# Kernel optimization log

Measured on AMD Instinct MI355X. Metric: run time of the kernel, lower is better.

The kernel has to match this reference:

```python
import jax, jax.numpy as jnp
import numpy as np

H, O, M, D, B = 4, 32, 128, 16, 1024
JITTER = 1e-4


def k_rbf(theta, X, Y):
    # theta: [H, 1+D] (log sf2, log lengthscales); X: [O,Mx,D]; Y: [O,My,D]
    sf2 = jnp.exp(theta[:, 0])[:, None, None, None]          # [H,1,1,1]
    ls = jnp.exp(theta[:, 1:])                               # [H,D]
    Xs = X[None] / ls[:, None, None, :]                      # [H,O,Mx,D]
    Ys = Y[None] / ls[:, None, None, :]                      # [H,O,My,D]
    d2 = ((Xs ** 2).sum(-1)[..., :, None]
          + (Ys ** 2).sum(-1)[..., None, :]
          - 2.0 * jnp.einsum('homd,hond->homn', Xs, Ys))
    return sf2 * jnp.exp(-0.5 * jnp.maximum(d2, 0.0))


def vec2tril(vec, m):
    r, c = jnp.tril_indices(m)
    L = jnp.zeros(vec.shape[:-1] + (m, m), vec.dtype)
    return L.at[..., r, c].set(vec)


def _st(Lmat, rhs):
    return jax.scipy.linalg.solve_triangular(Lmat, rhs, lower=True)


def setup_inputs() -> dict:
    key = jax.random.key(0)
    ks = jax.random.split(key, 8)
    eye = jnp.eye(M, dtype=jnp.float32)
    return {
        'x': jax.random.normal(ks[0], (B, D), jnp.float32),
        'z': 0.5 * jax.random.normal(ks[1], (O, M, D), jnp.float32),
        'u_mean': 0.5 * jax.random.normal(ks[2], (O, M, 1), jnp.float32),
        'u_tril_vec': 0.1 * jax.random.normal(ks[3], (O, M * (M + 1) // 2), jnp.float32),
        'm_old': 0.5 * jax.random.normal(ks[4], (O, M, 1), jnp.float32),
        'L_old': jnp.tril(0.1 * jax.random.normal(ks[5], (O, M, M), jnp.float32)) + eye,
        'z_old': 0.5 * jax.random.normal(ks[6], (O, M, D), jnp.float32),
        'theta': 0.1 * jax.random.normal(ks[7], (H, D + 1), jnp.float32),
    }


def reference(x, z, u_mean, u_tril_vec, m_old, L_old, z_old, theta):
    dt = x.dtype
    u_tril = vec2tril(u_tril_vec, M)                          # [O,M,M]
    eyeM = jnp.eye(M, dtype=dt)

    # ---- linear_gauss_joint (one previous task) ----
    kuf = k_rbf(theta, z_old, z)                              # [H,O,M,M]
    kuu = k_rbf(theta, z_old, z_old)                          # [H,O,M,M]
    Lkuu = jnp.linalg.cholesky(kuu + JITTER * eyeM)
    LKinvKuf = _st(Lkuu, kuf)
    m_oldh = jnp.broadcast_to(m_old[None], (H, O, M, 1))
    L_oldh = jnp.broadcast_to(L_old[None], (H, O, M, M))
    LKinvm = _st(Lkuu, m_oldh)
    Am = jnp.einsum('...ij,...ik->...jk', LKinvKuf, LKinvm)   # A @ m_old, [H,O,M,1]
    m_new = Am + u_mean[None]
    m_joint = jnp.concatenate([m_oldh, m_new], axis=-2)       # [H,O,2M,1]

    S_old = jnp.einsum('...ji,...ki->...jk', L_oldh, L_oldh)
    LKinvLS = _st(Lkuu, L_oldh)
    AtX = jnp.einsum('...ij,...ik->...jk', LKinvLS, LKinvKuf)  # [H,O,M,M]
    SoldAt = jnp.einsum('...ji,...ik->...jk', L_oldh, AtX)
    ASoldt = jnp.swapaxes(SoldAt, -1, -2)
    S_cur = jnp.einsum('...ji,...ki->...jk', u_tril, u_tril)[None]
    ASoldAt = jnp.einsum('...ij,...ik->...jk', AtX, AtX)
    cov_joint = jnp.concatenate([
        jnp.concatenate([S_old, SoldAt], axis=-1),
        jnp.concatenate([ASoldt, S_cur + ASoldAt], axis=-1)], axis=-2)
    eye2M = jnp.eye(2 * M, dtype=dt)
    L_joint = jnp.linalg.cholesky(cov_joint + JITTER * eye2M)  # [H,O,2M,2M]
    z_joint = jnp.concatenate([z_old, z], axis=-2)             # [O,2M,D]

    # ---- linear_gauss_conditional_diag ----
    xb = jnp.broadcast_to(x[None], (O, B, D))
    kuf2 = k_rbf(theta, z_joint, xb)                           # [H,O,2M,B]
    kuu2 = k_rbf(theta, z_joint, z_joint)
    Lk2 = jnp.linalg.cholesky(kuu2 + JITTER * eye2M)
    LKinvu = _st(Lk2, m_joint)
    LKinvKuf2 = _st(Lk2, kuf2)
    kff_diag = jnp.exp(theta[:, 0])[:, None, None]             # [H,1,1]
    diag1 = (LKinvKuf2 ** 2).sum(axis=-2)                      # [H,O,B]
    LKinvLs = _st(Lk2, L_joint)
    vec2 = jnp.einsum('...ij,...ik->...jk', LKinvLs, LKinvKuf2)
    diag2 = (vec2 ** 2).sum(axis=-2)
    mu = jnp.einsum('...ij,...ik->...jk', LKinvKuf2, LKinvu)[..., 0]
    var = kff_diag - diag1 + diag2
    return mu, var
```

## Files before the change

kernel.cpp:

```cpp
#include <hip/hip_runtime.h>

#define H_ 4
#define O_ 32
#define HO 128
#define M_ 128
#define M2 256
#define D_ 16
#define B_ 1024
#define JIT 1e-4f

typedef unsigned short ushort_t;
typedef __bf16 v8bf __attribute__((ext_vector_type(8)));
typedef float v16f __attribute__((ext_vector_type(16)));
typedef unsigned short v8us __attribute__((ext_vector_type(8)));
typedef unsigned short v4us __attribute__((ext_vector_type(4)));

__device__ inline void splitbf(float v, ushort_t& hb, ushort_t& lb) {
    unsigned int u = __float_as_uint(v);
    hb = (ushort_t)(u >> 16);
    float hf = __uint_as_float((unsigned int)hb << 16);
    float r = v - hf;
    lb = (ushort_t)(__float_as_uint(r) >> 16);
}
__device__ inline float bf2f(ushort_t u) { return __uint_as_float((unsigned int)u << 16); }

__device__ __forceinline__ float rdlane(float v, int l) {
    return __int_as_float(__builtin_amdgcn_readlane(__float_as_int(v), l));
}

__device__ __forceinline__ int ro_(int i) {
    int M = i >> 2, k = i & 3;
    return 4 * (M + 1) * (2 * M + k);
}

__global__ __launch_bounds__(256) void k_prekuu2(const float* __restrict__ theta,
                                                 const float* __restrict__ x,
                                                 const float* __restrict__ z,
                                                 const float* __restrict__ z_old,
                                                 float* __restrict__ SF2,
                                                 float* __restrict__ XS, float* __restrict__ XN,
                                                 float* __restrict__ ZS, float* __restrict__ ZN,
                                                 float* __restrict__ K2) {
    int bb = blockIdx.x, t = threadIdx.x;
    __shared__ float zs[M2][D_];
    __shared__ float zn[M2];
    __shared__ float ls[D_];
    if (bb == 272) {
        if (t < H_) SF2[t] = __expf(theta[t * (D_ + 1)]);
        return;
    }
    if (bb >= 256) {
        int j = (bb - 256) * 256 + t;
        int h = j >> 10, b = j & 1023;
        if (t < D_) ls[t] = __expf(-theta[h * (D_ + 1) + 1 + t]);
        __syncthreads();
        float s = 0.f;
#pragma unroll
        for (int d = 0; d < D_; d++) {
            float v = x[b * D_ + d] * ls[d];
            XS[(long)j * D_ + d] = v;
            s += v * v;
        }
        XN[j] = s;
        return;
    }
    int pair = bb >> 1, half = bb & 1;
    int h = pair >> 5, o = pair & 31, i = t;
    if (t < D_) ls[t] = __expf(-theta[h * (D_ + 1) + 1 + t]);
    __syncthreads();
    const float* src = (i < M_) ? (z_old + ((long)o * M_ + i) * D_)
                                : (z + ((long)o * M_ + (i - M_)) * D_);
    float s = 0.f;
#pragma unroll
    for (int d = 0; d < D_; d++) {
        float v = src[d] * ls[d];
        zs[i][d] = v;
        if (half == 0) ZS[((long)pair * M2 + i) * D_ + d] = v;
        s += v * v;
    }
    zn[i] = s;
    if (half == 0) ZN[pair * M2 + i] = s;
    __syncthreads();
    float sf2 = __expf(theta[h * (D_ + 1)]);
    float my[D_];
#pragma unroll
    for (int d = 0; d < D_; d++) my[d] = zs[i][d];
    float myn = zn[i];
    int q0 = half * 128;
    for (int q = q0; q < q0 + 128; q++) {
        float dot = 0.f;
#pragma unroll
        for (int d = 0; d < D_; d++) dot += zs[q][d] * my[d];
        float d2 = fmaxf(zn[q] + myn - 2.f * dot, 0.f);
        float v = sf2 * __expf(-0.5f * d2);
        if (q == i) v += JIT;
        K2[(long)pair * M2 * M2 + (long)q * M2 + i] = v;
    }
}

#define AP_SZ 8448
#define LV_SZ 16896
#define WS_SZ 4608
#define TM_SZ 3456
#define SH_TOTAL (AP_SZ + LV_SZ + WS_SZ + TM_SZ + 128)

__device__ __forceinline__ void choltri_body(const float* __restrict__ S, int ldsrc,
                                             float* __restrict__ Li, long b1, int t,
                                             float* __restrict__ Ap, float* __restrict__ Lv,
                                             float* __restrict__ Ws4, float* __restrict__ Tm,
                                             float* __restrict__ rdia) {
#pragma unroll
    for (int u = 0; u < 16; u++) {
        int idx = u * 256 + t;
        int i = idx >> 5, jc = (idx & 31) * 4;
        float4 v = *(const float4*)(S + (long)i * ldsrc + jc);
        int tb = ro_(i) + jc;
        if (jc + 3 <= i) {
            *(float4*)&Ap[tb] = v;
        } else if (jc <= i) {
            Ap[tb] = v.x;
            if (jc + 1 <= i) Ap[tb + 1] = v.y;
            if (jc + 2 <= i) Ap[tb + 2] = v.z;
        }
    }
    __syncthreads();

    int lane = t & 63;
    int wav = t >> 6;
    int r = lane & 31;

    for (int kb = 0; kb < 4; kb++) {
        int c0 = kb * 32;
        if (wav == 0) {
            float a[32];
            int gr = c0 + r;
            int base = ro_(gr) + c0;
#pragma unroll
            for (int j = 0; j < 32; j++) a[j] = Ap[base + j];
#pragma unroll
            for (int k = 0; k < 32; k++) {
                float dk = rdlane(a[k], k);
                float rs = rsqrtf(dk);
                rs = rs * (1.5f - 0.5f * dk * rs * rs);
                a[k] *= rs;
                if (lane == k) rdia[c0 + k] = rs;
#pragma unroll
                for (int j = k + 1; j < 32; j++) {
                    float ljk = rdlane(a[k], j);
                    a[j] = fmaf(-a[k], ljk, a[j]);
                }
            }
            if (lane < 32) {
#pragma unroll
                for (int j = 0; j < 32; j++)
                    if (j <= r) Ap[base + j] = a[j];
            }
        }
        __syncthreads();
        int R = 96 - c0;
        if (R > 0) {
            if (t < R) {
                int gi = c0 + 32 + t;
                int pb = ro_(gi) + c0;
                float xr[32];
#pragma unroll
                for (int j = 0; j < 32; j++) xr[j] = Ap[pb + j];
#pragma unroll
                for (int q = 0; q < 32; q++) {
                    float xq = xr[q] * rdia[c0 + q];
                    xr[q] = xq;
#pragma unroll
                    for (int j = q + 1; j < 32; j++)
                        xr[j] = fmaf(-xq, Ap[ro_(c0 + j) + c0 + q], xr[j]);
                }
#pragma unroll
                for (int j = 0; j < 32; j++) Ap[pb + j] = xr[j];
            }
            __syncthreads();
            int nb = R >> 2;
            int ntile = nb * (nb + 1) / 2;
            for (int tp = t; tp < ntile; tp += 256) {
                int bi = (int)((sqrtf(8.f * tp + 1.f) - 1.f) * 0.5f);
                while ((bi + 1) * (bi + 2) / 2 <= tp) bi++;
                while (bi * (bi + 1) / 2 > tp) bi--;
                int bj = tp - bi * (bi + 1) / 2;
                int i0 = c0 + 32 + bi * 4, j0 = c0 + 32 + bj * 4;
                int ra[4], rb[4];
#pragma unroll
                for (int q = 0; q < 4; q++) {
                    ra[q] = ro_(i0 + q) + c0;
                    rb[q] = ro_(j0 + q) + c0;
                }
                float acc[4][4] = {};
#pragma unroll
                for (int k4 = 0; k4 < 8; k4++) {
                    float4 av[4], bv[4];
#pragma unroll
                    for (int q = 0; q < 4; q++) {
                        av[q] = *(const float4*)&Ap[ra[q] + k4 * 4];
                        bv[q] = *(const float4*)&Ap[rb[q] + k4 * 4];
                    }
#pragma unroll
                    for (int q = 0; q < 4; q++)
#pragma unroll
                        for (int rr = 0; rr < 4; rr++)
                            acc[q][rr] += av[q].x * bv[rr].x + av[q].y * bv[rr].y +
                                          av[q].z * bv[rr].z + av[q].w * bv[rr].w;
                }
#pragma unroll
                for (int q = 0; q < 4; q++)
#pragma unroll
                    for (int rr = 0; rr < 4; rr++) {
                        int gi = i0 + q, gj = j0 + rr;
                        if (gj <= gi) Ap[ro_(gi) + gj] -= acc[q][rr];
                    }
            }
            __syncthreads();
        }
    }

    {
        int pb = wav;
        int c0 = pb * 32;
        float a[32];
        int gr = c0 + r;
        int base = ro_(gr) + c0;
#pragma unroll
        for (int j = 0; j < 32; j++) a[j] = Ap[base + j];
        float wr[32];
#pragma unroll
        for (int i = 0; i < 32; i++) {
            float rdi = rdia[c0 + i];
            float acc = 0.f;
#pragma unroll
            for (int j = 0; j < i; j++) {
                float lij = rdlane(a[j], i);
                acc = fmaf(lij, wr[j], acc);
            }
            wr[i] = (i == r) ? rdi : -acc * rdi;
        }
        if (lane < 32) {
            float* Wp = Ws4 + pb * 1152;
#pragma unroll
            for (int i = 0; i < 32; i++) Wp[i * 36 + r] = wr[i];
        }
    }
    __syncthreads();

    for (int e = t; e < 4096; e += 256) {
        int i = e >> 5, j = (e & 31) * 4;
        int bi = i >> 5, bj = j >> 5;
        float4 v = make_float4(0.f, 0.f, 0.f, 0.f);
        if (bi == bj) v = *(const float4*)&Ws4[bi * 1152 + (i & 31) * 36 + (j & 31)];
        *(float4*)&Lv[i * 132 + j] = v;
    }
    __syncthreads();
    for (int d = 1; d < 4; d++) {
        int nblk = 4 - d;
        int ne = nblk * 256;
        for (int p = t; p < ne; p += 256) {
            int b = p >> 8, rc = p & 255;
            int rr = rc >> 3, c4 = (rc & 7) * 4;
            int ib = b + d;
            int abase = ro_(ib * 32 + rr);
            float4 acc = make_float4(0.f, 0.f, 0.f, 0.f);
            for (int k = b; k < ib; k++) {
                const float* Arow = Ap + abase + k * 32;
                const float* L0 = Lv + (k * 32) * 132 + b * 32 + c4;
#pragma unroll
                for (int q4 = 0; q4 < 8; q4++) {
                    float4 ar = *(const float4*)(Arow + q4 * 4);
                    const float* Lq = L0 + (q4 * 4) * 132;
                    float4 l0 = *(const float4*)(Lq);
                    float4 l1 = *(const float4*)(Lq + 132);
                    float4 l2 = *(const float4*)(Lq + 264);
                    float4 l3 = *(const float4*)(Lq + 396);
                    acc.x += ar.x * l0.x + ar.y * l1.x + ar.z * l2.x + ar.w * l3.x;
                    acc.y += ar.x * l0.y + ar.y * l1.y + ar.z * l2.y + ar.w * l3.y;
                    acc.z += ar.x * l0.z + ar.y * l1.z + ar.z * l2.z + ar.w * l3.z;
                    acc.w += ar.x * l0.w + ar.y * l1.w + ar.z * l2.w + ar.w * l3.w;
                }
            }
            *(float4*)(Tm + b * 1152 + rr * 36 + c4) = acc;
        }
        __syncthreads();
        for (int p = t; p < ne; p += 256) {
            int b = p >> 8, rc = p & 255;
            int rr = rc >> 3, c4 = (rc & 7) * 4;
            int ib = b + d;
            const float* Wp = Ws4 + ib * 1152 + rr * 36;
            const float* T0 = Tm + b * 1152 + c4;
            float4 acc = make_float4(0.f, 0.f, 0.f, 0.f);
#pragma unroll
            for (int q4 = 0; q4 < 8; q4++) {
                float4 w4 = *(const float4*)(Wp + q4 * 4);
                const float* Tq = T0 + (q4 * 4) * 36;
                float4 t0 = *(const float4*)(Tq);
                float4 t1 = *(const float4*)(Tq + 36);
                float4 t2 = *(const float4*)(Tq + 72);
                float4 t3 = *(const float4*)(Tq + 108);
                acc.x += w4.x * t0.x + w4.y * t1.x + w4.z * t2.x + w4.w * t3.x;
                acc.y += w4.x * t0.y + w4.y * t1.y + w4.z * t2.y + w4.w * t3.y;
                acc.z += w4.x * t0.z + w4.y * t1.z + w4.z * t2.z + w4.w * t3.z;
                acc.w += w4.x * t0.w + w4.y * t1.w + w4.z * t2.w + w4.w * t3.w;
            }
            *(float4*)(Lv + (ib * 32 + rr) * 132 + b * 32 + c4) =
                make_float4(-acc.x, -acc.y, -acc.z, -acc.w);
        }
        __syncthreads();
    }
#pragma unroll
    for (int u = 0; u < 16; u++) {
        int idx = u * 256 + t;
        int i = idx >> 5, jc = (idx & 31) * 4;
        *(float4*)(Li + b1 + (long)i * 128 + jc) = *(const float4*)(Lv + i * 132 + jc);
    }
}

__global__ __launch_bounds__(256) void k_choltri_tl(const float* __restrict__ src,
                                                    float* __restrict__ Li,
                                                    const float* __restrict__ L_old,
                                                    const float* __restrict__ vec,
                                                    ushort_t* __restrict__ WTh,
                                                    ushort_t* __restrict__ WTl) {
    int bb = blockIdx.x, t = threadIdx.x;
    __shared__ __align__(16) float SH[SH_TOTAL];
    if (bb < 128) {
        choltri_body(src + (long)bb * ((long)M2 * M2), M2, Li, (long)bb * 16384, t,
                     SH, SH + AP_SZ, SH + AP_SZ + LV_SZ, SH + AP_SZ + LV_SZ + WS_SZ,
                     SH + AP_SZ + LV_SZ + WS_SZ + TM_SZ);
        return;
    }
    int pair = bb - 128, o = pair & 31;
    long b2 = (long)pair * 65536;
    float* vs = SH;
    float(*tile)[33] = (float(*)[33])(SH + AP_SZ);
    for (int e = t; e < M_ * (M_ + 1) / 2; e += 256) vs[e] = vec[(long)o * (M_ * (M_ + 1) / 2) + e];
    __syncthreads();
    for (int e = t; e < 16384; e += 256) {
        int n = e >> 7, k = e & 127;
        float v = (k >= n) ? vs[k * (k + 1) / 2 + n] : 0.f;
        ushort_t hb, lb;
        splitbf(v, hb, lb);
        long a = b2 + (long)(128 + n) * 256 + 128 + k;
        WTh[a] = hb;
        WTl[a] = lb;
    }
    for (int e = t; e < 16384; e += 256) {
        int n = e >> 7, k = e & 127;
        long a = b2 + (long)(128 + n) * 256 + k;
        WTh[a] = 0;
        WTl[a] = 0;
    }
    const float* sp = L_old + (long)o * 16384;
    int tx = t & 31, ty = t >> 5;
    for (int bi = 0; bi < 4; bi++)
        for (int bj = 0; bj < 4; bj++) {
            __syncthreads();
            for (int r = ty; r < 32; r += 8)
                tile[r][tx] = sp[(long)(bi * 32 + r) * 128 + bj * 32 + tx];
            __syncthreads();
            for (int r = ty; r < 32; r += 8) {
                ushort_t hb, lb;
                splitbf(tile[tx][r], hb, lb);
                long a = b2 + (long)(bj * 32 + r) * 256 + bi * 32 + tx;
                WTh[a] = hb;
                WTl[a] = lb;
            }
        }
}

__global__ __launch_bounds__(256) void k_choltri_br(const float* __restrict__ src,
                                                    float* __restrict__ Li,
                                                    const float* __restrict__ A1,
                                                    const float* __restrict__ Linv1,
                                                    float* __restrict__ T1g,
                                                    const float* __restrict__ BLW,
                                                    ushort_t* __restrict__ LTh,
                                                    ushort_t* __restrict__ LTl,
                                                    ushort_t* __restrict__ WTh,
                                                    ushort_t* __restrict__ WTl) {
    int bb = blockIdx.x, t = threadIdx.x;
    __shared__ __align__(16) float SH[SH_TOTAL];
    if (bb < 128) {
        choltri_body(src + (long)bb * ((long)M2 * M2), M2, Li, (long)bb * 16384, t,
                     SH, SH + AP_SZ, SH + AP_SZ + LV_SZ, SH + AP_SZ + LV_SZ + WS_SZ,
                     SH + AP_SZ + LV_SZ + WS_SZ + TM_SZ);
        return;
    }
    if (bb < 256) {
        int pair = bb - 128;
        long b1 = (long)pair * 16384;
        float(*As)[132] = (float(*)[132])(SH + AP_SZ);
        float(*Bs)[132] = ((float(*)[132])(SH + AP_SZ)) + 16;
        const float* Apt = A1 + b1;
        const float* Bpt = Linv1 + b1;
        float* Cp = T1g + (long)pair * 65536;
        int tx = t & 15, ty = t >> 4;
        float acc[8][8] = {};
        for (int kt = 0; kt < M_; kt += 16) {
#pragma unroll
            for (int q = 0; q < 8; q++) {
                int e = q * 256 + t;
                int kk = e >> 7, m = e & 127;
                As[kk][m] = Apt[(long)(kt + kk) * 128 + m];
                Bs[kk][m] = Bpt[(long)(kt + kk) * 128 + m];
            }
            __syncthreads();
#pragma unroll
            for (int kk = 0; kk < 16; kk++) {
                float a[8], b[8];
#pragma unroll
                for (int q = 0; q < 8; q++) { a[q] = As[kk][ty + 16 * q]; b[q] = Bs[kk][tx + 16 * q]; }
#pragma unroll
                for (int q = 0; q < 8; q++)
#pragma unroll
                    for (int r = 0; r < 8; r++) acc[q][r] += a[q] * b[r];
            }
            __syncthreads();
        }
#pragma unroll
        for (int q = 0; q < 8; q++)
#pragma unroll
            for (int r = 0; r < 8; r++)
                Cp[(long)(ty + 16 * q) * 128 + tx + 16 * r] = acc[q][r];
        return;
    }
    if (bb < 384) {
        int pair = bb - 256;
        long b2 = (long)pair * 65536, b1 = (long)pair * 16384;
        float(*tile)[33] = (float(*)[33])(SH + AP_SZ);
        for (int e = t; e < 16384; e += 256) {
            int n = e >> 7, k = e & 127;
            long a = b2 + (long)(128 + n) * 256 + k;
            LTh[a] = 0;
            LTl[a] = 0;
        }
        const float* sp = Linv1 + b1;
        int tx = t & 31, ty = t >> 5;
        for (int bi = 0; bi < 4; bi++)
            for (int bj = 0; bj < 4; bj++) {
                __syncthreads();
                for (int r = ty; r < 32; r += 8)
                    tile[r][tx] = sp[(long)(bi * 32 + r) * 128 + bj * 32 + tx];
                __syncthreads();
                for (int r = ty; r < 32; r += 8) {
                    ushort_t hb, lb;
                    splitbf(tile[tx][r], hb, lb);
                    long a = b2 + (long)(bj * 32 + r) * 256 + bi * 32 + tx;
                    LTh[a] = hb;
                    LTl[a] = lb;
                }
            }
        return;
    }
    {
        int pair = bb - 384;
        long b2 = (long)pair * 65536, b1 = (long)pair * 16384;
        float(*tile)[33] = (float(*)[33])(SH + AP_SZ);
        const float* sp = BLW + b1;
        int tx = t & 31, ty = t >> 5;
        for (int bi = 0; bi < 4; bi++)
            for (int bj = 0; bj < 4; bj++) {
                __syncthreads();
                for (int r = ty; r < 32; r += 8)
                    tile[r][tx] = sp[(long)(bi * 32 + r) * 128 + bj * 32 + tx];
                __syncthreads();
                for (int r = ty; r < 32; r += 8) {
                    ushort_t hb, lb;
                    splitbf(tile[tx][r], hb, lb);
                    long a = b2 + (long)(bj * 32 + r) * 256 + 128 + bi * 32 + tx;
                    WTh[a] = hb;
                    WTl[a] = lb;
                }
            }
    }
}

__global__ __launch_bounds__(256) void k_a1a3(const float* __restrict__ Linv1,
                                              const float* __restrict__ KUU2,
                                              const float* __restrict__ L_old,
                                              float* __restrict__ A1, float* __restrict__ A3) {
    int pair = blockIdx.x, y = blockIdx.y, o = pair & 31;
    const float* Ap = Linv1 + (long)pair * 16384;
    const float* Bp = y ? (L_old + (long)o * 16384) : (KUU2 + (long)pair * 65536 + 128);
    int ldb = y ? 128 : 256;
    float* Cp = (y ? A3 : A1) + (long)pair * 16384;
    int t = threadIdx.x, tx = t & 15, ty = t >> 4;
    __shared__ float As[16][132], Bs[16][132];
    float acc[8][8] = {};
    for (int kt = 0; kt < M_; kt += 16) {
#pragma unroll
        for (int q = 0; q < 8; q++) {
            int e = q * 256 + t;
            int m = e >> 4, kk = e & 15;
            As[kk][m] = Ap[(long)m * 128 + kt + kk];
            int kk2 = e >> 7, n = e & 127;
            Bs[kk2][n] = Bp[(long)(kt + kk2) * ldb + n];
        }
        __syncthreads();
#pragma unroll
        for (int kk = 0; kk < 16; kk++) {
            float a[8], b[8];
#pragma unroll
            for (int q = 0; q < 8; q++) { a[q] = As[kk][ty + 16 * q]; b[q] = Bs[kk][tx + 16 * q]; }
#pragma unroll
            for (int q = 0; q < 8; q++)
#pragma unroll
                for (int r = 0; r < 8; r++) acc[q][r] += a[q] * b[r];
        }
        __syncthreads();
    }
#pragma unroll
    for (int q = 0; q < 8; q++)
#pragma unroll
        for (int r = 0; r < 8; r++)
            Cp[(long)(ty + 16 * q) * 128 + tx + 16 * r] = acc[q][r];
}

__global__ __launch_bounds__(256) void k_blwschur(const float* __restrict__ A1,
                                                  const float* __restrict__ A3,
                                                  float* __restrict__ BLW,
                                                  float* __restrict__ KUU2,
                                                  const float* __restrict__ Linv1,
                                                  const float* __restrict__ m_old,
                                                  const float* __restrict__ u_mean,
                                                  float* __restrict__ MJ,
                                                  float* __restrict__ CV) {
    int pair = blockIdx.x, y = blockIdx.y, o = pair & 31;
    int t = threadIdx.x;
    if (y == 2) {
        CV[pair * 256 + t] = 0.f;
        __shared__ float mo[128], a2[128];
        if (t < 128) mo[t] = m_old[o * 128 + t];
        __syncthreads();
        if (t < 128) {
            const float* Lr = Linv1 + (long)pair * 16384 + (long)t * 128;
            float acc = 0.f;
            for (int j = 0; j <= t; j++) acc += Lr[j] * mo[j];
            a2[t] = acc;
        }
        __syncthreads();
        if (t < 128) {
            float m = 0.f;
            for (int i = 0; i < 128; i++) m += A1[(long)pair * 16384 + (long)i * 128 + t] * a2[i];
            MJ[pair * 256 + t] = mo[t];
            MJ[pair * 256 + 128 + t] = m + u_mean[o * 128 + t];
        }
        return;
    }
    const float* Ap = A1 + (long)pair * 16384;
    const float* Bp = (y ? A1 : A3) + (long)pair * 16384;
    float* Cp;
    int ldc;
    if (y) { Cp = KUU2 + (long)pair * 65536 + 128L * 256 + 128; ldc = 256; }
    else   { Cp = BLW + (long)pair * 16384; ldc = 128; }
    int tx = t & 15, ty = t >> 4;
    __shared__ float As[16][132], Bs[16][132];
    float acc[8][8] = {};
    for (int kt = 0; kt < M_; kt += 16) {
#pragma unroll
        for (int q = 0; q < 8; q++) {
            int e = q * 256 + t;
            int kk = e >> 7, m = e & 127;
            As[kk][m] = Ap[(long)(kt + kk) * 128 + m];
            Bs[kk][m] = Bp[(long)(kt + kk) * 128 + m];
        }
        __syncthreads();
#pragma unroll
        for (int kk = 0; kk < 16; kk++) {
            float a[8], b[8];
#pragma unroll
            for (int q = 0; q < 8; q++) { a[q] = As[kk][ty + 16 * q]; b[q] = Bs[kk][tx + 16 * q]; }
#pragma unroll
            for (int q = 0; q < 8; q++)
#pragma unroll
                for (int r = 0; r < 8; r++) acc[q][r] += a[q] * b[r];
        }
        __syncthreads();
    }
#pragma unroll
    for (int q = 0; q < 8; q++)
#pragma unroll
        for (int r = 0; r < 8; r++) {
            long idx = (long)(ty + 16 * q) * ldc + tx + 16 * r;
            if (y) Cp[idx] -= acc[q][r];
            else Cp[idx] = acc[q][r];
        }
}

__global__ __launch_bounds__(256) void k_blicalc2(const float* __restrict__ Linv2,
                                                  const float* __restrict__ T1g,
                                                  ushort_t* __restrict__ LTh,
                                                  ushort_t* __restrict__ LTl) {
    int pair = blockIdx.x, y = blockIdx.y;
    int t = threadIdx.x, tx = t & 15, ty = t >> 4;
    long b1 = (long)pair * 16384, b2 = (long)pair * 65536;
    int m0 = y * 64;
    __shared__ float T1s[64][129];
    __shared__ float As[16][68], Bs[16][132];
    const float* Apt = Linv2 + b1;
    const float* Bpt = T1g + (long)pair * 65536;
    float acc[4][8] = {};
    for (int kt = 0; kt < M_; kt += 16) {
#pragma unroll
        for (int q = 0; q < 4; q++) {
            int e = q * 256 + t;
            int m = e >> 4, kk = e & 15;
            As[kk][m] = Apt[(long)(m0 + m) * 128 + kt + kk];
        }
#pragma unroll
        for (int q = 0; q < 8; q++) {
            int e = q * 256 + t;
            int kk2 = e >> 7, n = e & 127;
            Bs[kk2][n] = Bpt[(long)(kt + kk2) * 128 + n];
        }
        __syncthreads();
#pragma unroll
        for (int kk = 0; kk < 16; kk++) {
            float a[4], b[8];
#pragma unroll
            for (int q = 0; q < 4; q++) a[q] = As[kk][ty + 16 * q];
#pragma unroll
            for (int r = 0; r < 8; r++) b[r] = Bs[kk][tx + 16 * r];
#pragma unroll
            for (int q = 0; q < 4; q++)
#pragma unroll
                for (int r = 0; r < 8; r++) acc[q][r] += a[q] * b[r];
        }
        __syncthreads();
    }
#pragma unroll
    for (int q = 0; q < 4; q++)
#pragma unroll
        for (int r = 0; r < 8; r++) T1s[ty + 16 * q][tx + 16 * r] = -acc[q][r];
    __syncthreads();
    for (int e = t; e < 8192; e += 256) {
        int j = e >> 6, i2 = e & 63;
        ushort_t hb, lb;
        splitbf(T1s[i2][j], hb, lb);
        long a = b2 + (long)j * 256 + 128 + m0 + i2;
        LTh[a] = hb;
        LTl[a] = lb;
    }
    __syncthreads();
    for (int e = t; e < 8192; e += 256) {
        int k2 = e >> 7, j = e & 127;
        T1s[k2][j] = Apt[(long)(m0 + k2) * 128 + j];
    }
    __syncthreads();
    for (int e = t; e < 8192; e += 256) {
        int n = e >> 6, k2 = e & 63;
        ushort_t hb, lb;
        splitbf(T1s[k2][n], hb, lb);
        long a = b2 + (long)(128 + n) * 256 + 128 + m0 + k2;
        LTh[a] = hb;
        LTl[a] = lb;
    }
}

#define BSTR 56
template <int TILES3>
__global__ __launch_bounds__(256) void k_bmmx(const ushort_t* __restrict__ Ah,
                                              const ushort_t* __restrict__ Al,
                                              const ushort_t* __restrict__ Bh,
                                              const ushort_t* __restrict__ Bl,
                                              float* __restrict__ Cf,
                                              ushort_t* __restrict__ Chi,
                                              ushort_t* __restrict__ Clo,
                                              const float* __restrict__ Dm,
                                              int kLoMode, float alpha,
                                              const float* __restrict__ MJv,
                                              float* __restrict__ CVat) {
    int pair = blockIdx.x;
    long base = (long)pair * 65536;
    int I0, J0, mir = 0;
    if (TILES3) {
        int qb = blockIdx.y;
        I0 = (qb == 0) ? 0 : 128;
        J0 = (qb == 2) ? 0 : I0;
        mir = (qb == 2);
    } else {
        I0 = (blockIdx.y >> 1) * 128;
        J0 = (blockIdx.y & 1) * 128;
    }
    int k0 = (kLoMode == 1) ? max(I0, J0) : (kLoMode == 2) ? J0 : 0;
    int t = threadIdx.x;
    int w = t >> 6, lane = t & 63;
    int l31 = lane & 31, lhalf = lane >> 5;
    int wy = w >> 1, wx = w & 1;

    __shared__ __align__(16) ushort_t AsH[128][BSTR], AsL[128][BSTR];
    __shared__ __align__(16) ushort_t BsH[128][BSTR], BsL[128][BSTR];

    v16f acc[2][2];
#pragma unroll
    for (int mt = 0; mt < 2; mt++)
#pragma unroll
        for (int nt = 0; nt < 2; nt++)
#pragma unroll
            for (int r = 0; r < 16; r++) acc[mt][nt][r] = 0.f;

    for (int kt = k0; kt < 256; kt += 32) {
        __syncthreads();
#pragma unroll
        for (int u = 0; u < 2; u++) {
            int idx = u * 256 + t;
            int m = idx >> 2, kc = (idx & 3) * 8;
            long arow = base + (long)(I0 + m) * 256 + kt + kc;
            long brow = base + (long)(J0 + m) * 256 + kt + kc;
            *(v8us*)&AsH[m][kc] = *(const v8us*)(Ah + arow);
            *(v8us*)&AsL[m][kc] = *(const v8us*)(Al + arow);
            *(v8us*)&BsH[m][kc] = *(const v8us*)(Bh + brow);
            *(v8us*)&BsL[m][kc] = *(const v8us*)(Bl + brow);
        }
        __syncthreads();
#pragma unroll
        for (int ks = 0; ks < 2; ks++) {
            int ko = ks * 16 + lhalf * 8;
            v8bf ah[2], al[2], bh[2], bl[2];
#pragma unroll
            for (int mt = 0; mt < 2; mt++) {
                int r = wy * 64 + mt * 32 + l31;
                ah[mt] = *(const v8bf*)&AsH[r][ko];
                al[mt] = *(const v8bf*)&AsL[r][ko];
            }
#pragma unroll
            for (int nt = 0; nt < 2; nt++) {
                int r = wx * 64 + nt * 32 + l31;
                bh[nt] = *(const v8bf*)&BsH[r][ko];
                bl[nt] = *(const v8bf*)&BsL[r][ko];
            }
#pragma unroll
            for (int mt = 0; mt < 2; mt++)
#pragma unroll
                for (int nt = 0; nt < 2; nt++) {
                    acc[mt][nt] = __builtin_amdgcn_mfma_f32_32x32x16_bf16(ah[mt], bh[nt], acc[mt][nt], 0, 0, 0);
                    acc[mt][nt] = __builtin_amdgcn_mfma_f32_32x32x16_bf16(ah[mt], bl[nt], acc[mt][nt], 0, 0, 0);
                    acc[mt][nt] = __builtin_amdgcn_mfma_f32_32x32x16_bf16(al[mt], bh[nt], acc[mt][nt], 0, 0, 0);
                }
        }
    }

    float mjc[2] = {0.f, 0.f};
    float cvmir[2] = {0.f, 0.f};
    if (MJv) {
#pragma unroll
        for (int nt = 0; nt < 2; nt++)
            mjc[nt] = MJv[(long)pair * 256 + J0 + wx * 64 + nt * 32 + l31];
    }
#pragma unroll
    for (int mt = 0; mt < 2; mt++) {
#pragma unroll
        for (int r = 0; r < 16; r++) {
            int row = I0 + wy * 64 + mt * 32 + 8 * (r >> 2) + 4 * lhalf + (r & 3);
            float rowsum = 0.f;
            float mjrow = 0.f;
            if (MJv && mir) mjrow = MJv[(long)pair * 256 + row];
#pragma unroll
            for (int nt = 0; nt < 2; nt++) {
                int col = J0 + wx * 64 + nt * 32 + l31;
                long idx = base + (long)row * 256 + col;
                float v = alpha * acc[mt][nt][r];
                if (Dm) v += Dm[idx];
                ushort_t hb, lb;
                splitbf(v, hb, lb);
                if (Cf) Cf[idx] = v;
                if (Chi) { Chi[idx] = hb; Clo[idx] = lb; }
                if (mir) {
                    long idxT = base + (long)col * 256 + row;
                    if (Cf) Cf[idxT] = v;
                    if (Chi) { Chi[idxT] = hb; Clo[idxT] = lb; }
                }
                if (MJv) {
                    rowsum += v * mjc[nt];
                    if (mir) cvmir[nt] += v * mjrow;
                }
            }
            if (MJv) {
#pragma unroll
                for (int m = 1; m < 32; m <<= 1) rowsum += __shfl_xor(rowsum, m, 64);
                if (l31 == 0) atomicAdd(&CVat[(long)pair * 256 + row], rowsum);
            }
        }
    }
    if (MJv && mir) {
#pragma unroll
        for (int nt = 0; nt < 2; nt++)
            atomicAdd(&CVat[(long)pair * 256 + J0 + wx * 64 + nt * 32 + l31], cvmir[nt]);
    }
}

#define KTP 280
__global__ __launch_bounds__(256) void k_kbuild(const float* __restrict__ ZS, const float* __restrict__ ZN,
                                                const float* __restrict__ XS, const float* __restrict__ XN,
                                                const float* __restrict__ SF2, const float* __restrict__ CV,
                                                ushort_t* __restrict__ Kg, float* __restrict__ out) {
    int bt = blockIdx.x;
    int pair = blockIdx.y;
    int h = pair >> 5;
    int t = threadIdx.x;
    int w = t >> 6;
    int b = t & 63;

    __shared__ __align__(16) ushort_t KbT[64][KTP];
    __shared__ float mup[4][64];

    const float LOG2E = 1.4426950408889634f;
    const float NHL = -0.5f * 1.4426950408889634f;
    float sf2 = SF2[h];
    float lsf2 = __log2f(sf2);
    long bg = (long)h * B_ + bt * 64 + b;
    const float4* xrow = (const float4*)(XS + bg * 16);
    float4 x0 = xrow[0], x1 = xrow[1], x2 = xrow[2], x3 = xrow[3];
    float bx = NHL * XN[bg];
    float mupart = 0.f;
    const float* cvp = CV + pair * 256;
    const float* znp = ZN + pair * 256;
#pragma unroll 2
    for (int j8 = 0; j8 < 8; j8++) {
        v8us kb8;
#pragma unroll
        for (int e = 0; e < 8; e++) {
            int j = w * 64 + j8 * 8 + e;
            const float4* zrow = (const float4*)(ZS + ((long)pair * 256 + j) * 16);
            float4 z0 = zrow[0], z1 = zrow[1], z2 = zrow[2], z3 = zrow[3];
            float dot = z0.x * x0.x + z0.y * x0.y + z0.z * x0.z + z0.w * x0.w +
                        z1.x * x1.x + z1.y * x1.y + z1.z * x1.z + z1.w * x1.w +
                        z2.x * x2.x + z2.y * x2.y + z2.z * x2.z + z2.w * x2.w +
                        z3.x * x3.x + z3.y * x3.y + z3.z * x3.z + z3.w * x3.w;
            float pre = fmaf(znp[j], NHL, fmaf(dot, LOG2E, bx));
            float wexp = fminf(pre, 0.f) + lsf2;
            float kv;
            asm("v_exp_f32 %0, %1" : "=v"(kv) : "v"(wexp));
            mupart += cvp[j] * kv;
            unsigned int u = __float_as_uint(kv);
            u += 0x7fffu + ((u >> 16) & 1u);
            kb8[e] = (unsigned short)(u >> 16);
        }
        *(v8us*)&KbT[b][w * 64 + j8 * 8] = kb8;
    }
    mup[w][b] = mupart;
    __syncthreads();
    long kbase = ((long)pair * 1024 + bt * 64) * 256;
#pragma unroll
    for (int e = 0; e < 8; e++) {
        int c = e * 256 + t;
        int bb = c >> 5, cj = (c & 31) * 8;
        *(v8us*)(Kg + kbase + (long)bb * 256 + cj) = *(const v8us*)&KbT[bb][cj];
    }
    if (t < 64) {
        float mu = mup[0][t] + mup[1][t] + mup[2][t] + mup[3][t];
        out[(long)pair * 1024 + bt * 64 + t] = mu;
    }
}

#define KT2 264
__global__ __launch_bounds__(256) void k_kb4(const ushort_t* __restrict__ Kg,
                                             const ushort_t* __restrict__ Ghi,
                                             const ushort_t* __restrict__ Glo,
                                             const float* __restrict__ SF2, float* __restrict__ out) {
    int pair = blockIdx.x & 127;
    int bt = blockIdx.x >> 7;
    int h = pair >> 5;
    int t = threadIdx.x;
    int w = t >> 6;
    int lane = t & 63;
    int l31 = lane & 31, lhalf = lane >> 5;

    __shared__ __align__(16) ushort_t KbT[128][KT2];
    __shared__ float qpart[4][128];

    float sf2 = SF2[h];
    long kbase = ((long)pair * 1024 + bt * 128) * 256;
#pragma unroll
    for (int e = 0; e < 16; e++) {
        int c = e * 256 + t;
        int bb = c >> 5, cj = (c & 31) * 8;
        *(v8us*)&KbT[bb][cj] = *(const v8us*)(Kg + kbase + (long)bb * 256 + cj);
    }
    __syncthreads();

    v16f acc[2][4];
#pragma unroll
    for (int mt = 0; mt < 2; mt++)
#pragma unroll
        for (int nt = 0; nt < 4; nt++)
#pragma unroll
            for (int r = 0; r < 16; r++) acc[mt][nt][r] = 0.f;

    const ushort_t* GhiP = Ghi + (long)pair * 65536;
    const ushort_t* GloP = Glo + (long)pair * 65536;
#pragma unroll 2
    for (int k0 = 0; k0 < 256; k0 += 16) {
        v8bf bfr[4];
#pragma unroll
        for (int nt = 0; nt < 4; nt++)
            bfr[nt] = *(const v8bf*)&KbT[nt * 32 + l31][k0 + lhalf * 8];
#pragma unroll
        for (int mt = 0; mt < 2; mt++) {
            int i = w * 64 + mt * 32 + l31;
            v8bf ah = *(const v8bf*)(GhiP + (long)i * 256 + k0 + lhalf * 8);
            v8bf al = *(const v8bf*)(GloP + (long)i * 256 + k0 + lhalf * 8);
#pragma unroll
            for (int nt = 0; nt < 4; nt++) {
                acc[mt][nt] = __builtin_amdgcn_mfma_f32_32x32x16_bf16(ah, bfr[nt], acc[mt][nt], 0, 0, 0);
                acc[mt][nt] = __builtin_amdgcn_mfma_f32_32x32x16_bf16(al, bfr[nt], acc[mt][nt], 0, 0, 0);
            }
        }
    }

    float qp[4] = {0.f, 0.f, 0.f, 0.f};
#pragma unroll
    for (int mt = 0; mt < 2; mt++) {
#pragma unroll
        for (int nt = 0; nt < 4; nt++) {
            int b = nt * 32 + l31;
#pragma unroll
            for (int g = 0; g < 4; g++) {
                int ibase = w * 64 + mt * 32 + 8 * g + 4 * lhalf;
                v4us k4 = *(const v4us*)&KbT[b][ibase];
#pragma unroll
                for (int e = 0; e < 4; e++) {
                    float kv = bf2f(k4[e]);
                    qp[nt] += kv * acc[mt][nt][4 * g + e];
                }
            }
        }
    }
#pragma unroll
    for (int nt = 0; nt < 4; nt++) {
        qp[nt] += __shfl_down(qp[nt], 32, 64);
        if (lhalf == 0) qpart[w][nt * 32 + l31] = qp[nt];
    }
    __syncthreads();

    if (t < 128) {
        float q = qpart[0][t] + qpart[1][t] + qpart[2][t] + qpart[3][t];
        out[(long)H_ * O_ * B_ + (long)pair * 1024 + bt * 128 + t] = sf2 - q;
    }
}

extern "C" void kernel_launch(void* const* d_in, const int* in_sizes, int n_in,
                              void* d_out, int out_size, void* d_ws, size_t ws_size,
                              hipStream_t stream) {
    const float* x = (const float*)d_in[0];
    const float* z = (const float*)d_in[1];
    const float* u_mean = (const float*)d_in[2];
    const float* u_tril_vec = (const float*)d_in[3];
    const float* m_old = (const float*)d_in[4];
    const float* L_old = (const float*)d_in[5];
    const float* z_old = (const float*)d_in[6];
    const float* theta = (const float*)d_in[7];

    const long BIGSZ = (long)HO * M2 * M2;
    const long MSZ = (long)HO * M_ * M_;

    float* ws = (float*)d_ws;
    long off = 0;
    float* BIG0 = ws + off; off += BIGSZ;
    float* BIG1 = ws + off; off += BIGSZ;
    float* BIG2 = ws + off; off += BIGSZ;
    float* BIG3 = ws + off; off += BIGSZ;
    float* ZS = ws + off; off += (long)HO * M2 * D_;
    float* XS = ws + off; off += (long)H_ * B_ * D_;
    float* ZN = ws + off; off += (long)HO * M2;
    float* XN = ws + off; off += (long)H_ * B_;
    float* MJ = ws + off; off += (long)HO * M2;
    float* CV = ws + off; off += (long)HO * M2;
    float* SF2v = ws + off; off += H_;

    float* KUU2 = BIG0;
    float* AINV = BIG0;
    float* T1g = BIG0;
    float* Linv1 = BIG2;
    float* A1 = BIG2 + MSZ;
    float* A3 = BIG2 + 2 * MSZ;
    float* Linv2 = BIG2 + 2 * MSZ;
    float* BLW = BIG2 + 3 * MSZ;
    ushort_t* LINVTh = (ushort_t*)BIG1;
    ushort_t* LINVTl = LINVTh + BIGSZ;
    ushort_t* AINVh = (ushort_t*)BIG2;
    ushort_t* AINVl = AINVh + BIGSZ;
    ushort_t* WcTh = (ushort_t*)BIG3;
    ushort_t* WcTl = WcTh + BIGSZ;
    ushort_t* Yh = (ushort_t*)BIG1;
    ushort_t* Yl = Yh + BIGSZ;
    ushort_t* Ghi = (ushort_t*)BIG3;
    ushort_t* Glo = Ghi + BIGSZ;
    ushort_t* Kg = (ushort_t*)BIG1;
    const long BRoff = 128L * M2 + 128;

    k_prekuu2<<<273, 256, 0, stream>>>(theta, x, z, z_old, SF2v, XS, XN, ZS, ZN, KUU2);
    k_choltri_tl<<<256, 256, 0, stream>>>(KUU2, Linv1, L_old, u_tril_vec, WcTh, WcTl);
    k_a1a3<<<dim3(HO, 2), 256, 0, stream>>>(Linv1, KUU2, L_old, A1, A3);
    k_blwschur<<<dim3(HO, 3), 256, 0, stream>>>(A1, A3, BLW, KUU2, Linv1, m_old, u_mean, MJ, CV);
    k_choltri_br<<<512, 256, 0, stream>>>(KUU2 + BRoff, Linv2, A1, Linv1, T1g, BLW,
                                          LINVTh, LINVTl, WcTh, WcTl);
    k_blicalc2<<<dim3(HO, 2), 256, 0, stream>>>(Linv2, T1g, LINVTh, LINVTl);
    k_bmmx<1><<<dim3(HO, 3), 256, 0, stream>>>(LINVTh, LINVTl, LINVTh, LINVTl,
                                               AINV, AINVh, AINVl, nullptr, 1, 1.f, MJ, CV);
    k_bmmx<0><<<dim3(HO, 4), 256, 0, stream>>>(AINVh, AINVl, WcTh, WcTl,
                                               nullptr, Yh, Yl, nullptr, 2, 1.f, nullptr, nullptr);
    k_bmmx<1><<<dim3(HO, 3), 256, 0, stream>>>(Yh, Yl, Yh, Yl,
                                               nullptr, Ghi, Glo, AINV, 0, -1.f, nullptr, nullptr);
    k_kbuild<<<dim3(16, HO), 256, 0, stream>>>(ZS, ZN, XS, XN, SF2v, CV, Kg, (float*)d_out);
    k_kb4<<<1024, 256, 0, stream>>>(Kg, Ghi, Glo, SF2v, (float*)d_out);
}
```

Before: 570.8 us.

## Fuse kernel-matrix build into quadratic-form MFMA kernel, dropping global Kg round-trip

New measurement: 605.2 us. 1.06x slower.

```diff
diff --git a/kernel.cpp b/kernel.cpp
--- a/kernel.cpp
+++ b/kernel.cpp
@@ -791,25 +791,30 @@
     }
 }
 
-#define KTP 280
-__global__ __launch_bounds__(256) void k_kbuild(const float* __restrict__ ZS, const float* __restrict__ ZN,
-                                                const float* __restrict__ XS, const float* __restrict__ XN,
-                                                const float* __restrict__ SF2, const float* __restrict__ CV,
-                                                ushort_t* __restrict__ Kg, float* __restrict__ out) {
-    int bt = blockIdx.x;
-    int pair = blockIdx.y;
+#define KT2 264
+__global__ __launch_bounds__(256) void k_kq2(const float* __restrict__ ZS, const float* __restrict__ ZN,
+                                             const float* __restrict__ XS, const float* __restrict__ XN,
+                                             const float* __restrict__ SF2, const float* __restrict__ CV,
+                                             const ushort_t* __restrict__ Ghi,
+                                             const ushort_t* __restrict__ Glo,
+                                             float* __restrict__ out) {
+    int pair = blockIdx.x & 127;
+    int bt = blockIdx.x >> 7;
     int h = pair >> 5;
     int t = threadIdx.x;
     int w = t >> 6;
-    int b = t & 63;
-
-    __shared__ __align__(16) ushort_t KbT[64][KTP];
-    __shared__ float mup[4][64];
+    int lane = t & 63;
+    int l31 = lane & 31, lhalf = lane >> 5;
+
+    __shared__ __align__(16) ushort_t KbT[64][KT2];
+    __shared__ float qpart[4][64];
 
     const float LOG2E = 1.4426950408889634f;
     const float NHL = -0.5f * 1.4426950408889634f;
     float sf2 = SF2[h];
     float lsf2 = __log2f(sf2);
+
+    int b = t & 63;
     long bg = (long)h * B_ + bt * 64 + b;
     const float4* xrow = (const float4*)(XS + bg * 16);
     float4 x0 = xrow[0], x1 = xrow[1], x2 = xrow[2], x3 = xrow[3];
@@ -840,52 +845,18 @@
         }
         *(v8us*)&KbT[b][w * 64 + j8 * 8] = kb8;
     }
-    mup[w][b] = mupart;
-    __syncthreads();
-    long kbase = ((long)pair * 1024 + bt * 64) * 256;
-#pragma unroll
-    for (int e = 0; e < 8; e++) {
-        int c = e * 256 + t;
-        int bb = c >> 5, cj = (c & 31) * 8;
-        *(v8us*)(Kg + kbase + (long)bb * 256 + cj) = *(const v8us*)&KbT[bb][cj];
-    }
-    if (t < 64) {
-        float mu = mup[0][t] + mup[1][t] + mup[2][t] + mup[3][t];
-        out[(long)pair * 1024 + bt * 64 + t] = mu;
-    }
-}
-
-#define KT2 264
-__global__ __launch_bounds__(256) void k_kb4(const ushort_t* __restrict__ Kg,
-                                             const ushort_t* __restrict__ Ghi,
-                                             const ushort_t* __restrict__ Glo,
-                                             const float* __restrict__ SF2, float* __restrict__ out) {
-    int pair = blockIdx.x & 127;
-    int bt = blockIdx.x >> 7;
-    int h = pair >> 5;
-    int t = threadIdx.x;
-    int w = t >> 6;
-    int lane = t & 63;
-    int l31 = lane & 31, lhalf = lane >> 5;
-
-    __shared__ __align__(16) ushort_t KbT[128][KT2];
-    __shared__ float qpart[4][128];
-
-    float sf2 = SF2[h];
-    long kbase = ((long)pair * 1024 + bt * 128) * 256;
-#pragma unroll
-    for (int e = 0; e < 16; e++) {
-        int c = e * 256 + t;
-        int bb = c >> 5, cj = (c & 31) * 8;
-        *(v8us*)&KbT[bb][cj] = *(const v8us*)(Kg + kbase + (long)bb * 256 + cj);
-    }
-    __syncthreads();
-
-    v16f acc[2][4];
+    qpart[w][b] = mupart;
+    __syncthreads();
+    if (t < 64)
+        out[(long)pair * 1024 + bt * 64 + t] =
+            qpart[0][t] + qpart[1][t] + qpart[2][t] + qpart[3][t];
+    __syncthreads();
+
+    v16f acc[2][2];
 #pragma unroll
     for (int mt = 0; mt < 2; mt++)
 #pragma unroll
-        for (int nt = 0; nt < 4; nt++)
+        for (int nt = 0; nt < 2; nt++)
 #pragma unroll
             for (int r = 0; r < 16; r++) acc[mt][nt][r] = 0.f;
 
@@ -893,9 +864,9 @@
     const ushort_t* GloP = Glo + (long)pair * 65536;
 #pragma unroll 2
     for (int k0 = 0; k0 < 256; k0 += 16) {
-        v8bf bfr[4];
-#pragma unroll
-        for (int nt = 0; nt < 4; nt++)
+        v8bf bfr[2];
+#pragma unroll
+        for (int nt = 0; nt < 2; nt++)
             bfr[nt] = *(const v8bf*)&KbT[nt * 32 + l31][k0 + lhalf * 8];
 #pragma unroll
         for (int mt = 0; mt < 2; mt++) {
@@ -903,23 +874,23 @@
             v8bf ah = *(const v8bf*)(GhiP + (long)i * 256 + k0 + lhalf * 8);
             v8bf al = *(const v8bf*)(GloP + (long)i * 256 + k0 + lhalf * 8);
 #pragma unroll
-            for (int nt = 0; nt < 4; nt++) {
+            for (int nt = 0; nt < 2; nt++) {
                 acc[mt][nt] = __builtin_amdgcn_mfma_f32_32x32x16_bf16(ah, bfr[nt], acc[mt][nt], 0, 0, 0);
                 acc[mt][nt] = __builtin_amdgcn_mfma_f32_32x32x16_bf16(al, bfr[nt], acc[mt][nt], 0, 0, 0);
             }
         }
     }
 
-    float qp[4] = {0.f, 0.f, 0.f, 0.f};
+    float qp[2] = {0.f, 0.f};
 #pragma unroll
     for (int mt = 0; mt < 2; mt++) {
 #pragma unroll
-        for (int nt = 0; nt < 4; nt++) {
-            int b = nt * 32 + l31;
+        for (int nt = 0; nt < 2; nt++) {
+            int bb = nt * 32 + l31;
 #pragma unroll
             for (int g = 0; g < 4; g++) {
                 int ibase = w * 64 + mt * 32 + 8 * g + 4 * lhalf;
-                v4us k4 = *(const v4us*)&KbT[b][ibase];
+                v4us k4 = *(const v4us*)&KbT[bb][ibase];
 #pragma unroll
                 for (int e = 0; e < 4; e++) {
                     float kv = bf2f(k4[e]);
@@ -929,15 +900,15 @@
         }
     }
 #pragma unroll
-    for (int nt = 0; nt < 4; nt++) {
+    for (int nt = 0; nt < 2; nt++) {
         qp[nt] += __shfl_down(qp[nt], 32, 64);
         if (lhalf == 0) qpart[w][nt * 32 + l31] = qp[nt];
     }
     __syncthreads();
 
-    if (t < 128) {
+    if (t < 64) {
         float q = qpart[0][t] + qpart[1][t] + qpart[2][t] + qpart[3][t];
-        out[(long)H_ * O_ * B_ + (long)pair * 1024 + bt * 128 + t] = sf2 - q;
+        out[(long)H_ * O_ * B_ + (long)pair * 1024 + bt * 64 + t] = sf2 - q;
     }
 }
 
@@ -988,7 +959,6 @@
     ushort_t* Yl = Yh + BIGSZ;
     ushort_t* Ghi = (ushort_t*)BIG3;
     ushort_t* Glo = Ghi + BIGSZ;
-    ushort_t* Kg = (ushort_t*)BIG1;
     const long BRoff = 128L * M2 + 128;
 
     k_prekuu2<<<273, 256, 0, stream>>>(theta, x, z, z_old, SF2v, XS, XN, ZS, ZN, KUU2);
@@ -1004,6 +974,5 @@
                                                nullptr, Yh, Yl, nullptr, 2, 1.f, nullptr, nullptr);
     k_bmmx<1><<<dim3(HO, 3), 256, 0, stream>>>(Yh, Yl, Yh, Yl,
                                                nullptr, Ghi, Glo, AINV, 0, -1.f, nullptr, nullptr);
-    k_kbuild<<<dim3(16, HO), 256, 0, stream>>>(ZS, ZN, XS, XN, SF2v, CV, Kg, (float*)d_out);
-    k_kb4<<<1024, 256, 0, stream>>>(Kg, Ghi, Glo, SF2v, (float*)d_out);
-}
+    k_kq2<<<2048, 256, 0, stream>>>(ZS, ZN, XS, XN, SF2v, CV, Ghi, Glo, (float*)d_out);
+}
```
